# Performance work log

Hardware: AMD Instinct MI355X
Metric: run time of the kernel (lower is better)

Reference implementation:

```python
import jax, jax.numpy as jnp
import numpy as np
from jax import lax

B = 32        # true batch size (groups)
C_IN = 64     # per-sample input channels
C_OUT = 64    # per-sample output channels
H = W = 256
KH = KW = 3


def setup_inputs() -> dict:
    key = jax.random.key(0)
    kx, kk = jax.random.split(key)
    # x folds the batch into channels: [1, B*C_in, H, W]
    x = jax.random.normal(kx, (1, B * C_IN, H, W), dtype=jnp.float32)
    # per-sample kernels stacked along output-filter axis: [B*C_out, C_in, kH, kW]
    kernels = jax.random.normal(kk, (B * C_OUT, C_IN, KH, KW), dtype=jnp.float32)
    return {"x": x, "kernels": kernels, "batch_size": B}


def reference(x, kernels, batch_size):
    # F.conv2d(x, kernels, stride=1, padding='same', groups=batch_size)
    # Grouped conv with feature_group_count = batch_size (one group per sample).
    out = lax.conv_general_dilated(
        x,
        kernels,
        window_strides=(1, 1),
        padding="SAME",
        feature_group_count=batch_size,
        dimension_numbers=("NCHW", "OIHW", "NCHW"),
    )
    return out
```

## Files before the change

### kernel.cpp

```cpp
#include <hip/hip_runtime.h>
#include <hip/hip_bf16.h>


typedef __bf16 bf16x8 __attribute__((ext_vector_type(8)));
typedef float  f32x4  __attribute__((ext_vector_type(4)));

#define NB 32
#define NH 256
#define NW 256
#define TILE_H 4
#define TILE_W 64
#define XROWS 6
#define XCOLS 68

__global__ void repack_weights_kernel(const float* __restrict__ wsrc,
                                      __bf16* __restrict__ pk) {
    int t = blockIdx.x * blockDim.x + threadIdx.x;
    if (t >= NB * 9 * 4 * 2 * 64) return;
    int lane = t & 63;
    int r = t >> 6;
    int kc = r & 1;  r >>= 1;
    int mt = r & 3;  r >>= 2;
    int tap = r % 9;
    int b   = r / 9;
    int co  = b * 64 + mt * 16 + (lane & 15);
    int ci0 = kc * 32 + (lane >> 4) * 8;
    bf16x8 v;
#pragma unroll
    for (int j = 0; j < 8; ++j) {
        v[j] = (__bf16)wsrc[(co * 64 + ci0 + j) * 9 + tap];
    }
    *reinterpret_cast<bf16x8*>(pk + (size_t)t * 8) = v;
}

__launch_bounds__(256)
__global__ void conv_mfma_kernel(const float* __restrict__ x,
                                 const __bf16* __restrict__ pk,
                                 float* __restrict__ out) {
    __shared__ __align__(16) __bf16 xs[XROWS * XCOLS * 32];

    const int orig = blockIdx.x;
    const int wg   = (orig & 7) * 1024 + (orig >> 3);
    const int b    = wg >> 8;
    const int by   = (wg >> 2) & 63;
    const int bx   = wg & 3;
    const int h0   = by * TILE_H;
    const int w0   = bx * TILE_W;

    const int tid  = threadIdx.x;
    const int wid  = tid >> 6;
    const int lane = tid & 63;
    const int nl   = lane & 15;
    const int kgrp = lane >> 4;

    const __bf16* pkb = pk + (size_t)b * 9 * 4096;

    bf16x8 af[4][4];
    auto load_af = [&](int g) {
        const int tap = (g >= 9) ? g - 9 : g;
        const int kc  = (g >= 9) ? 1 : 0;
        const int sl  = g & 3;
#pragma unroll
        for (int mt = 0; mt < 4; ++mt)
            af[sl][mt] = *reinterpret_cast<const bf16x8*>(
                pkb + tap * 4096 + ((mt * 2 + kc) * 64 + lane) * 8);
    };

    load_af(0);
    load_af(1);

    f32x4 acc[4][4];
#pragma unroll
    for (int mt = 0; mt < 4; ++mt)
#pragma unroll
        for (int q = 0; q < 4; ++q)
            acc[mt][q] = (f32x4){0.f, 0.f, 0.f, 0.f};

    const int c    = lane;
    const int w    = w0 - 1 + c;
    const int wcl  = min(max(w, 0), NW - 1);
    const bool wbad = (w != wcl);
    const int sciw = ((wid ^ ((c >> 1) & 3)) * 8);

    const int hidx  = tid;
    const int hr    = hidx >> 3;
    const int hside = (hidx >> 2) & 1;
    const int hoct  = hidx & 3;
    const int hch   = 64 + hside;
    const int hw    = w0 + 63 + hside;
    const int hwc   = min(hw, NW - 1);

#pragma unroll
    for (int kc = 0; kc < 2; ++kc) {
        {
            const int cibase = b * 64 + kc * 32 + wid * 8;
            const float* colp = x + (size_t)cibase * NH * NW + wcl;

            float hv[8];
            if (tid < 48) {
                const int h  = h0 - 1 + hr;
                const int hc = min(max(h, 0), NH - 1);
                const float* src = x + ((size_t)(b * 64 + kc * 32 + hoct * 8) * NH + hc) * NW + hwc;
#pragma unroll
                for (int j = 0; j < 8; ++j) hv[j] = src[(size_t)j * NH * NW];
                if (h != hc || hw != hwc) {
#pragma unroll
                    for (int j = 0; j < 8; ++j) hv[j] = 0.f;
                }
            }

            float va[8], vb[8];
            auto load8 = [&](int r, float* v) {
                const int h  = h0 - 1 + r;
                const int hc = min(max(h, 0), NH - 1);
                const float* src = colp + (size_t)hc * NW;
#pragma unroll
                for (int j = 0; j < 8; ++j) v[j] = src[(size_t)j * NH * NW];
                if (wbad || h != hc) {
#pragma unroll
                    for (int j = 0; j < 8; ++j) v[j] = 0.f;
                }
            };
            auto store8 = [&](int r, const float* v) {
                bf16x8 o;
#pragma unroll
                for (int j = 0; j < 8; ++j) o[j] = (__bf16)v[j];
                *reinterpret_cast<bf16x8*>(xs + (r * XCOLS + c) * 32 + sciw) = o;
            };

            load8(0, va);
            load8(1, vb);
            store8(0, va); load8(2, va);
            store8(1, vb); load8(3, vb);
            store8(2, va); load8(4, va);
            store8(3, vb); load8(5, vb);
            store8(4, va);
            store8(5, vb);

            if (tid < 48) {
                bf16x8 o;
#pragma unroll
                for (int j = 0; j < 8; ++j) o[j] = (__bf16)hv[j];
                *reinterpret_cast<bf16x8*>(xs + (hr * XCOLS + hch) * 32 + hoct * 8) = o;
            }
        }
        __syncthreads();

#pragma unroll
        for (int tap = 0; tap < 9; ++tap) {
            const int g = kc * 9 + tap;
            if (g + 2 < 18) load_af(g + 2);
            const int kh = tap / 3;
            const int kw = tap - kh * 3;
            const int rowbase = (wid + kh) * XCOLS;
            const int fs = g & 3;
#pragma unroll
            for (int q = 0; q < 4; ++q) {
                const int cc   = q * 16 + nl + kw;
                const int slot = (cc >> 1) & 3;
                bf16x8 bfv = *reinterpret_cast<const bf16x8*>(
                    xs + (rowbase + cc) * 32 + ((kgrp ^ slot) * 8));
#pragma unroll
                for (int mt = 0; mt < 4; ++mt)
                    acc[mt][q] = __builtin_amdgcn_mfma_f32_16x16x32_bf16(
                        af[fs][mt], bfv, acc[mt][q], 0, 0, 0);
            }
        }
        if (kc == 0) __syncthreads();
    }

    const int mrow = kgrp * 4;
    const int h = h0 + wid;
#pragma unroll
    for (int mt = 0; mt < 4; ++mt) {
#pragma unroll
        for (int q = 0; q < 4; ++q) {
            const int ww = w0 + q * 16 + nl;
#pragma unroll
            for (int rg = 0; rg < 4; ++rg) {
                const int co = mt * 16 + mrow + rg;
                out[((size_t)(b * 64 + co) * NH + h) * NW + ww] = acc[mt][q][rg];
            }
        }
    }
}

extern "C" void kernel_launch(void* const* d_in, const int* in_sizes, int n_in,
                              void* d_out, int out_size, void* d_ws, size_t ws_size,
                              hipStream_t stream) {
    const float* x = (const float*)d_in[0];
    const float* w = (const float*)d_in[1];
    float* out = (float*)d_out;
    __bf16* pk = (__bf16*)d_ws;

    {
        int total = NB * 9 * 4 * 2 * 64;
        int blk = 256;
        int grid = (total + blk - 1) / blk;
        hipLaunchKernelGGL(repack_weights_kernel, dim3(grid), dim3(blk), 0, stream,
                           w, pk);
    }
    {
        dim3 grid(8192);
        hipLaunchKernelGGL(conv_mfma_kernel, grid, dim3(256), 0, stream,
                           x, pk, out);
    }
}
```

Baseline: 311.6 us.

## Stage weight fragments in LDS via global_load_lds instead of per-wave register prefetch

Each block now cooperatively loads the 36 weight fragments for the current channel half into shared memory with direct global-to-LDS loads, split across the four waves. Each wave then reads its A operands from LDS per tap. Before, every wave fetched the full weight set from global memory into registers. This removes redundant global weight traffic and frees registers, at the cost of 36 KB of extra LDS per block, which may reduce occupancy. It also depends on the existing barrier to order the async LDS writes before they are read.

```diff
diff --git a/kernel.cpp b/kernel.cpp
--- a/kernel.cpp
+++ b/kernel.cpp
@@ -12,6 +12,13 @@
 #define TILE_W 64
 #define XROWS 6
 #define XCOLS 68
+#define HWSZ ((size_t)NH * NW)
+
+__device__ __forceinline__ void gload16(const float* g, float* lds) {
+    __builtin_amdgcn_global_load_lds(
+        (const __attribute__((address_space(1))) unsigned int*)g,
+        (__attribute__((address_space(3))) unsigned int*)lds, 16, 0, 0);
+}
 
 __global__ void repack_weights_kernel(const float* __restrict__ wsrc,
                                       __bf16* __restrict__ pk) {
@@ -38,6 +45,7 @@
                                  const __bf16* __restrict__ pk,
                                  float* __restrict__ out) {
     __shared__ __align__(16) __bf16 xs[XROWS * XCOLS * 32];
+    __shared__ __align__(16) __bf16 afs[36 * 512];
 
     const int orig = blockIdx.x;
     const int wg   = (orig & 7) * 1024 + (orig >> 3);
@@ -53,21 +61,19 @@
     const int nl   = lane & 15;
     const int kgrp = lane >> 4;
 
-    const __bf16* pkb = pk + (size_t)b * 9 * 4096;
-
-    bf16x8 af[4][4];
-    auto load_af = [&](int g) {
-        const int tap = (g >= 9) ? g - 9 : g;
-        const int kc  = (g >= 9) ? 1 : 0;
-        const int sl  = g & 3;
-#pragma unroll
-        for (int mt = 0; mt < 4; ++mt)
-            af[sl][mt] = *reinterpret_cast<const bf16x8*>(
-                pkb + tap * 4096 + ((mt * 2 + kc) * 64 + lane) * 8);
+    const char* pkb = (const char*)(pk + (size_t)b * 9 * 4096);
+
+    auto issue_af = [&](int kcv) {
+#pragma unroll
+        for (int i = 0; i < 9; ++i) {
+            const int f  = wid * 9 + i;
+            const int tp = f >> 2;
+            const int mt = f & 3;
+            const float* src = (const float*)(pkb + tp * 8192
+                                              + (mt * 2 + kcv) * 1024 + lane * 16);
+            gload16(src, (float*)((char*)afs + f * 1024));
+        }
     };
-
-    load_af(0);
-    load_af(1);
 
     f32x4 acc[4][4];
 #pragma unroll
@@ -82,10 +88,9 @@
     const bool wbad = (w != wcl);
     const int sciw = ((wid ^ ((c >> 1) & 3)) * 8);
 
-    const int hidx  = tid;
-    const int hr    = hidx >> 3;
-    const int hside = (hidx >> 2) & 1;
-    const int hoct  = hidx & 3;
+    const int hr    = tid >> 3;
+    const int hside = (tid >> 2) & 1;
+    const int hoct  = tid & 3;
     const int hch   = 64 + hside;
     const int hw    = w0 + 63 + hside;
     const int hwc   = min(hw, NW - 1);
@@ -93,8 +98,10 @@
 #pragma unroll
     for (int kc = 0; kc < 2; ++kc) {
         {
+            issue_af(kc);
+
             const int cibase = b * 64 + kc * 32 + wid * 8;
-            const float* colp = x + (size_t)cibase * NH * NW + wcl;
+            const float* colp = x + (size_t)cibase * HWSZ + wcl;
 
             float hv[8];
             if (tid < 48) {
@@ -102,7 +109,7 @@
                 const int hc = min(max(h, 0), NH - 1);
                 const float* src = x + ((size_t)(b * 64 + kc * 32 + hoct * 8) * NH + hc) * NW + hwc;
 #pragma unroll
-                for (int j = 0; j < 8; ++j) hv[j] = src[(size_t)j * NH * NW];
+                for (int j = 0; j < 8; ++j) hv[j] = src[j * HWSZ];
                 if (h != hc || hw != hwc) {
 #pragma unroll
                     for (int j = 0; j < 8; ++j) hv[j] = 0.f;
@@ -115,7 +122,7 @@
                 const int hc = min(max(h, 0), NH - 1);
                 const float* src = colp + (size_t)hc * NW;
 #pragma unroll
-                for (int j = 0; j < 8; ++j) v[j] = src[(size_t)j * NH * NW];
+                for (int j = 0; j < 8; ++j) v[j] = src[j * HWSZ];
                 if (wbad || h != hc) {
 #pragma unroll
                     for (int j = 0; j < 8; ++j) v[j] = 0.f;
@@ -148,12 +155,14 @@
 
 #pragma unroll
         for (int tap = 0; tap < 9; ++tap) {
-            const int g = kc * 9 + tap;
-            if (g + 2 < 18) load_af(g + 2);
+            bf16x8 afr[4];
+#pragma unroll
+            for (int mt = 0; mt < 4; ++mt)
+                afr[mt] = *reinterpret_cast<const bf16x8*>(
+                    afs + (tap * 4 + mt) * 512 + lane * 8);
             const int kh = tap / 3;
             const int kw = tap - kh * 3;
             const int rowbase = (wid + kh) * XCOLS;
-            const int fs = g & 3;
 #pragma unroll
             for (int q = 0; q < 4; ++q) {
                 const int cc   = q * 16 + nl + kw;
@@ -163,7 +172,7 @@
 #pragma unroll
                 for (int mt = 0; mt < 4; ++mt)
                     acc[mt][q] = __builtin_amdgcn_mfma_f32_16x16x32_bf16(
-                        af[fs][mt], bfv, acc[mt][q], 0, 0, 0);
+                        afr[mt], bfv, acc[mt][q], 0, 0, 0);
             }
         }
         if (kc == 0) __syncthreads();
```

After: 289.4 us (median of 2 runs). 1.08x faster.
